# Optimization experiments

Measured on AMD Instinct MI355X. Metric: run time of the kernel, lower is better.

The kernel has to match this reference:

```python
import jax, jax.numpy as jnp
import numpy as np

D_MODEL = 256; N_HEADS = 8; HEAD_DIM = 32; N_LEVELS = 4; N_POINTS = 4; N_LAYERS = 3; D_FFN = 1024
SHAPES = np.array([[76, 76], [38, 38], [19, 19], [10, 10]], dtype=np.int64)
S_TOTAL = int((SHAPES[:, 0] * SHAPES[:, 1]).sum())  # 7681


def setup_inputs():
    key = jax.random.key(0)
    ks = jax.random.split(key, 12)
    B = 1; C = D_MODEL; M = N_HEADS; Lv = N_LEVELS; P = N_POINTS; L = N_LAYERS; s = 0.02
    starts = np.concatenate([[0], np.cumsum(SHAPES[:, 0] * SHAPES[:, 1])[:-1]]).astype(np.int64)
    inp = {
        "src": jax.random.normal(ks[0], (B, S_TOTAL, C), jnp.float32),
        "pos": jax.random.normal(ks[1], (B, S_TOTAL, C), jnp.float32),
        "valid_ratios": jnp.ones((B, Lv, 2), jnp.float32),
        "spatial_shapes": jnp.asarray(SHAPES),
        "level_start_index": jnp.asarray(starts),
        "padding_mask": jnp.zeros((B, S_TOTAL), bool),
        "W_off": jax.random.normal(ks[2], (L, C, M * Lv * P * 2), jnp.float32) * s,
        "b_off": jax.random.normal(ks[3], (L, M * Lv * P * 2), jnp.float32) * s,
        "W_attn": jax.random.normal(ks[4], (L, C, M * Lv * P), jnp.float32) * s,
        "b_attn": jax.random.normal(ks[5], (L, M * Lv * P), jnp.float32) * s,
        "W_val": jax.random.normal(ks[6], (L, C, C), jnp.float32) * s,
        "b_val": jnp.zeros((L, C), jnp.float32),
        "W_out": jax.random.normal(ks[7], (L, C, C), jnp.float32) * s,
        "b_out": jnp.zeros((L, C), jnp.float32),
        "ln1_g": jnp.ones((L, C), jnp.float32),
        "ln1_b": jnp.zeros((L, C), jnp.float32),
        "W_ff1": jax.random.normal(ks[8], (L, C, D_FFN), jnp.float32) * s,
        "b_ff1": jnp.zeros((L, D_FFN), jnp.float32),
        "W_ff2": jax.random.normal(ks[9], (L, D_FFN, C), jnp.float32) * s,
        "b_ff2": jnp.zeros((L, C), jnp.float32),
        "ln2_g": jnp.ones((L, C), jnp.float32),
        "ln2_b": jnp.zeros((L, C), jnp.float32),
    }
    return inp


def _ln(x, g, b):
    mu = x.mean(-1, keepdims=True)
    var = ((x - mu) ** 2).mean(-1, keepdims=True)
    return (x - mu) * jax.lax.rsqrt(var + 1e-5) * g + b


def _gather(v, idx):
    # v: [B, HW, M, D], idx: [B, S, M, P] -> [B, S, M, P, D], head-specific gather
    B, S, M, P = idx.shape
    def one(vb, ib):
        i2 = ib.transpose(0, 2, 1).reshape(S * P, M, 1)
        o = jnp.take_along_axis(vb, i2, axis=0)  # [S*P, M, D]
        return o.reshape(S, P, M, -1).transpose(0, 2, 1, 3)
    return jax.vmap(one)(v, idx)


def _msda(query, src, mask, ref, shapes, starts, Wo, bo, Wa, ba, Wv, bv, Wout, bout):
    # Multi-scale deformable attention (Deformable-DETR), grid_sample align_corners=False + zero padding
    B, S, C = src.shape
    M, Lv, P, D = N_HEADS, N_LEVELS, N_POINTS, HEAD_DIM
    value = src @ Wv + bv
    value = jnp.where(mask[..., None], 0.0, value).reshape(B, S, M, D)
    off = (query @ Wo + bo).reshape(B, S, M, Lv, P, 2)
    aw = jax.nn.softmax((query @ Wa + ba).reshape(B, S, M, Lv * P), -1).reshape(B, S, M, Lv, P)
    norm = jnp.asarray(shapes[:, ::-1].copy(), jnp.float32)  # (W, H) per level
    loc = ref[:, :, None, :, None, :] + off / norm[None, None, None, :, None, :]  # [B,S,M,Lv,P,2]
    out = jnp.zeros((B, S, M, D), query.dtype)
    for lvl in range(Lv):
        H = int(shapes[lvl, 0]); W = int(shapes[lvl, 1]); st = int(starts[lvl])
        v = value[:, st:st + H * W]  # [B, H*W, M, D]
        l = loc[:, :, :, lvl]  # [B, S, M, P, 2]
        x = l[..., 0] * W - 0.5
        y = l[..., 1] * H - 0.5
        x0 = jnp.floor(x); y0 = jnp.floor(y)
        dx = x - x0; dy = y - y0
        samp = jnp.zeros((B, S, M, P, D), query.dtype)
        for yy, xx, w in ((y0, x0, (1 - dy) * (1 - dx)), (y0, x0 + 1, (1 - dy) * dx),
                          (y0 + 1, x0, dy * (1 - dx)), (y0 + 1, x0 + 1, dy * dx)):
            valid = (xx >= 0) & (xx < W) & (yy >= 0) & (yy < H)
            xi = jnp.clip(xx, 0, W - 1).astype(jnp.int32)
            yi = jnp.clip(yy, 0, H - 1).astype(jnp.int32)
            g = _gather(v, yi * W + xi)
            samp = samp + (w * valid)[..., None] * g
        out = out + (aw[:, :, :, lvl, :, None] * samp).sum(3)
    return out.reshape(B, S, C) @ Wout + bout


def _ref_points(vr, shapes):
    refs = []
    for lvl in range(shapes.shape[0]):
        H = int(shapes[lvl, 0]); W = int(shapes[lvl, 1])
        ry, rx = np.meshgrid(np.linspace(0.5, H - 0.5, H, dtype=np.float32),
                             np.linspace(0.5, W - 0.5, W, dtype=np.float32), indexing="ij")
        rxj = jnp.asarray(rx.reshape(-1))[None] / (vr[:, None, lvl, 0] * W)
        ryj = jnp.asarray(ry.reshape(-1))[None] / (vr[:, None, lvl, 1] * H)
        refs.append(jnp.stack([rxj, ryj], -1))
    ref = jnp.concatenate(refs, 1)  # [B, S, 2]
    return ref[:, :, None] * vr[:, None]  # [B, S, Lv, 2]


def _encoder(src, pos, valid_ratios, shapes, starts, mask, params):
    (W_off, b_off, W_attn, b_attn, W_val, b_val, W_out, b_out,
     ln1_g, ln1_b, W_ff1, b_ff1, W_ff2, b_ff2, ln2_g, ln2_b) = params
    ref = _ref_points(valid_ratios, shapes)
    out = src
    for l in range(N_LAYERS):
        q = out + pos  # with_pos_embed
        a = _msda(q, out, mask, ref, shapes, starts, W_off[l], b_off[l], W_attn[l], b_attn[l],
                  W_val[l], b_val[l], W_out[l], b_out[l])
        out = _ln(out + a, ln1_g[l], ln1_b[l])
        f = jax.nn.relu(out @ W_ff1[l] + b_ff1[l]) @ W_ff2[l] + b_ff2[l]
        out = _ln(out + f, ln2_g[l], ln2_b[l])
    return out


def reference(src, pos, valid_ratios, spatial_shapes, level_start_index, padding_mask,
              W_off, b_off, W_attn, b_attn, W_val, b_val, W_out, b_out,
              ln1_g, ln1_b, W_ff1, b_ff1, W_ff2, b_ff2, ln2_g, ln2_b):
    shapes = np.asarray(spatial_shapes)
    starts = np.asarray(level_start_index)
    params = (W_off, b_off, W_attn, b_attn, W_val, b_val, W_out, b_out,
              ln1_g, ln1_b, W_ff1, b_ff1, W_ff2, b_ff2, ln2_g, ln2_b)
    return _encoder(src, pos, valid_ratios, shapes, starts, padding_mask, params)
```

## Files before the change

### kernel.cpp

```cpp
#include <hip/hip_runtime.h>
#include <hip/hip_bf16.h>
#include <math.h>

#define S_TOTAL 7681

typedef __attribute__((ext_vector_type(8))) short bf16x8;
typedef __attribute__((ext_vector_type(4))) float f32x4;

__device__ __forceinline__ short f2b(float x) {
    union { float f; unsigned u; } v; v.f = x;
    unsigned r = v.u + 0x7FFFu + ((v.u >> 16) & 1u);
    return (short)(r >> 16);
}
__device__ __forceinline__ float b2f(unsigned short u) {
    union { unsigned u; float f; } t; t.u = ((unsigned)u) << 16; return t.f;
}

__global__ __launch_bounds__(256) void transpose_cvt_kernel(
    const float* __restrict__ s0, const float* __restrict__ s1,
    const float* __restrict__ s2, const float* __restrict__ s3,
    const float* __restrict__ s4, const float* __restrict__ s5,
    short* __restrict__ d0, short* __restrict__ d1, short* __restrict__ d2,
    short* __restrict__ d3, short* __restrict__ d4, short* __restrict__ d5)
{
    const int z = blockIdx.z;
    int t = blockIdx.x;
    const float* src; short* dst; int K, N, lt;
    if (t < 64)       { src = s0 + (size_t)z * 65536;  dst = d0 + (size_t)z * 65536;  K = 256;  N = 256;  lt = t; }
    else if (t < 128) { src = s1 + (size_t)z * 65536;  dst = d1 + (size_t)z * 98304;  K = 256;  N = 256;  lt = t - 64; }
    else if (t < 160) { src = s2 + (size_t)z * 32768;  dst = d2 + (size_t)z * 98304;  K = 256;  N = 128;  lt = t - 128; }
    else if (t < 224) { src = s3 + (size_t)z * 65536;  dst = d3 + (size_t)z * 65536;  K = 256;  N = 256;  lt = t - 160; }
    else if (t < 480) { src = s4 + (size_t)z * 262144; dst = d4 + (size_t)z * 262144; K = 256;  N = 1024; lt = t - 224; }
    else              { src = s5 + (size_t)z * 262144; dst = d5 + (size_t)z * 262144; K = 1024; N = 256;  lt = t - 480; }
    const int ntx = N >> 5;
    const int tk = (lt / ntx) << 5, tn = (lt % ntx) << 5;
    __shared__ float tile[32][33];
    const int cx = threadIdx.x & 31, cy = threadIdx.x >> 5;
    #pragma unroll
    for (int i = 0; i < 32; i += 8)
        tile[cy + i][cx] = src[(size_t)(tk + cy + i) * N + tn + cx];
    __syncthreads();
    #pragma unroll
    for (int i = 0; i < 32; i += 8)
        dst[(size_t)(tn + cy + i) * K + tk + cx] = f2b(tile[cx][cy + i]);
}

__global__ void bias_cat_kernel(const float* __restrict__ b_off,
                                const float* __restrict__ b_attn,
                                float* __restrict__ b_oa) {
    int l = blockIdx.x, i = threadIdx.x;
    b_oa[l * 384 + i] = (i < 256) ? b_off[l * 256 + i] : b_attn[l * 128 + (i - 256)];
}

#define BM 128
#define BN 64
#define BK 32
#define KP 40

template<int RELU, int OUTBF>
__global__ __launch_bounds__(256) void gemm_kernel(
    const short* __restrict__ A, const short* __restrict__ Wt,
    const float* __restrict__ bias, void* __restrict__ Cv,
    int M, int N, int K)
{
    __shared__ __align__(16) short As[BM * KP];
    __shared__ __align__(16) short Bs[BN * KP];
    const int tid = threadIdx.x;
    const int lane = tid & 63;
    const int wave = tid >> 6;
    const int rowBase = blockIdx.x * BM;
    const int colBase = blockIdx.y * BN;

    const int ar = tid >> 1;
    const int ak = (tid & 1) * 16;
    const int br = tid >> 2;
    const int bk = (tid & 3) * 8;

    const int frow = lane & 15;
    const int fko  = (lane >> 4) * 8;
    const int wm = wave * 32;

    f32x4 acc[2][4] = {};

    const int aRow = rowBase + ar;
    const bool aOk = aRow < M;
    const short* Ap = A + (size_t)aRow * K + ak;
    const short* Bp = Wt + (size_t)(colBase + br) * K + bk;

    bf16x8 a0 = {}, a1 = {}, b0 = {};
    if (aOk) { a0 = *(const bf16x8*)Ap; a1 = *(const bf16x8*)(Ap + 8); }
    b0 = *(const bf16x8*)Bp;

    for (int k0 = 0; k0 < K; k0 += BK) {
        *(bf16x8*)&As[ar * KP + ak]     = a0;
        *(bf16x8*)&As[ar * KP + ak + 8] = a1;
        *(bf16x8*)&Bs[br * KP + bk]     = b0;
        __syncthreads();

        const int kn = k0 + BK;
        if (kn < K) {
            if (aOk) { a0 = *(const bf16x8*)(Ap + kn); a1 = *(const bf16x8*)(Ap + kn + 8); }
            b0 = *(const bf16x8*)(Bp + kn);
        }

        bf16x8 af0 = *(const bf16x8*)&As[(wm + frow) * KP + fko];
        bf16x8 af1 = *(const bf16x8*)&As[(wm + 16 + frow) * KP + fko];
        #pragma unroll
        for (int j = 0; j < 4; ++j) {
            bf16x8 bfj = *(const bf16x8*)&Bs[(j * 16 + frow) * KP + fko];
            acc[0][j] = __builtin_amdgcn_mfma_f32_16x16x32_bf16(af0, bfj, acc[0][j], 0, 0, 0);
            acc[1][j] = __builtin_amdgcn_mfma_f32_16x16x32_bf16(af1, bfj, acc[1][j], 0, 0, 0);
        }
        __syncthreads();
    }

    const int erow = (lane >> 4) * 4;
    const int ecol = lane & 15;
    #pragma unroll
    for (int mi = 0; mi < 2; ++mi) {
        #pragma unroll
        for (int j = 0; j < 4; ++j) {
            #pragma unroll
            for (int r = 0; r < 4; ++r) {
                int row = rowBase + wm + mi * 16 + erow + r;
                if (row < M) {
                    int col = colBase + j * 16 + ecol;
                    float v = acc[mi][j][r] + bias[col];
                    if (RELU) v = fmaxf(v, 0.f);
                    if (OUTBF) ((short*)Cv)[(size_t)row * N + col] = f2b(v);
                    else       ((float*)Cv)[(size_t)row * N + col] = v;
                }
            }
        }
    }
}

template<int WRITEQ>
__global__ __launch_bounds__(256) void gemm_ln_kernel(
    const short* __restrict__ A, const short* __restrict__ Wt,
    const float* __restrict__ bias, const float* __restrict__ g,
    const float* __restrict__ bln, const float* __restrict__ pos,
    float* __restrict__ out, short* __restrict__ xb, short* __restrict__ qb,
    int M, int K)
{
    __shared__ __align__(16) short As[32 * KP];
    __shared__ __align__(16) short Bs[256 * KP];
    __shared__ float rsum[32][4], rsq[32][4], smu[32], srs[32];

    const int tid = threadIdx.x;
    const int lane = tid & 63;
    const int wave = tid >> 6;
    const int rowBase = blockIdx.x * 32;

    const int frow = lane & 15;
    const int fko  = (lane >> 4) * 8;

    f32x4 acc[2][4] = {};

    const int ar = tid >> 1;
    const int ak = (tid & 1) * 16;
    const int aRow = rowBase + ar;
    const bool aOk = (tid < 64) && (aRow < M);
    const short* Ap = A + (size_t)aRow * K + ak;
    const short* Bp = Wt + (size_t)tid * K;

    bf16x8 a0 = {}, a1 = {};
    bf16x8 w0, w1, w2, w3;
    if (aOk) { a0 = *(const bf16x8*)Ap; a1 = *(const bf16x8*)(Ap + 8); }
    w0 = *(const bf16x8*)(Bp);      w1 = *(const bf16x8*)(Bp + 8);
    w2 = *(const bf16x8*)(Bp + 16); w3 = *(const bf16x8*)(Bp + 24);

    for (int k0 = 0; k0 < K; k0 += BK) {
        if (tid < 64) {
            *(bf16x8*)&As[ar * KP + ak]     = a0;
            *(bf16x8*)&As[ar * KP + ak + 8] = a1;
        }
        *(bf16x8*)&Bs[tid * KP + 0]  = w0;
        *(bf16x8*)&Bs[tid * KP + 8]  = w1;
        *(bf16x8*)&Bs[tid * KP + 16] = w2;
        *(bf16x8*)&Bs[tid * KP + 24] = w3;
        __syncthreads();

        const int kn = k0 + BK;
        if (kn < K) {
            if (aOk) { a0 = *(const bf16x8*)(Ap + kn); a1 = *(const bf16x8*)(Ap + kn + 8); }
            w0 = *(const bf16x8*)(Bp + kn);      w1 = *(const bf16x8*)(Bp + kn + 8);
            w2 = *(const bf16x8*)(Bp + kn + 16); w3 = *(const bf16x8*)(Bp + kn + 24);
        }

        bf16x8 af0 = *(const bf16x8*)&As[frow * KP + fko];
        bf16x8 af1 = *(const bf16x8*)&As[(16 + frow) * KP + fko];
        #pragma unroll
        for (int j = 0; j < 4; ++j) {
            bf16x8 bfj = *(const bf16x8*)&Bs[(wave * 64 + j * 16 + frow) * KP + fko];
            acc[0][j] = __builtin_amdgcn_mfma_f32_16x16x32_bf16(af0, bfj, acc[0][j], 0, 0, 0);
            acc[1][j] = __builtin_amdgcn_mfma_f32_16x16x32_bf16(af1, bfj, acc[1][j], 0, 0, 0);
        }
        __syncthreads();
    }

    const int erow = (lane >> 4) * 4;
    const int ecol = lane & 15;
    float x[2][4][4];
    #pragma unroll
    for (int mi = 0; mi < 2; ++mi)
        #pragma unroll
        for (int j = 0; j < 4; ++j)
            #pragma unroll
            for (int r = 0; r < 4; ++r) {
                int row = rowBase + mi * 16 + erow + r;
                int col = wave * 64 + j * 16 + ecol;
                float res = (row < M) ? out[(size_t)row * 256 + col] : 0.f;
                x[mi][j][r] = acc[mi][j][r] + bias[col] + res;
            }

    #pragma unroll
    for (int mi = 0; mi < 2; ++mi)
        #pragma unroll
        for (int r = 0; r < 4; ++r) {
            float s1 = x[mi][0][r] + x[mi][1][r] + x[mi][2][r] + x[mi][3][r];
            float s2 = x[mi][0][r]*x[mi][0][r] + x[mi][1][r]*x[mi][1][r]
                     + x[mi][2][r]*x[mi][2][r] + x[mi][3][r]*x[mi][3][r];
            #pragma unroll
            for (int o = 1; o < 16; o <<= 1) {
                s1 += __shfl_xor(s1, o);
                s2 += __shfl_xor(s2, o);
            }
            if ((lane & 15) == 0) {
                rsum[mi * 16 + erow + r][wave] = s1;
                rsq [mi * 16 + erow + r][wave] = s2;
            }
        }
    __syncthreads();
    if (tid < 32) {
        float S1 = rsum[tid][0] + rsum[tid][1] + rsum[tid][2] + rsum[tid][3];
        float S2 = rsq[tid][0] + rsq[tid][1] + rsq[tid][2] + rsq[tid][3];
        float mu = S1 * (1.f / 256.f);
        smu[tid] = mu;
        srs[tid] = rsqrtf(S2 * (1.f / 256.f) - mu * mu + 1e-5f);
    }
    __syncthreads();

    #pragma unroll
    for (int mi = 0; mi < 2; ++mi)
        #pragma unroll
        for (int r = 0; r < 4; ++r) {
            int lrow = mi * 16 + erow + r;
            int row = rowBase + lrow;
            if (row >= M) continue;
            float mu = smu[lrow], rs = srs[lrow];
            #pragma unroll
            for (int j = 0; j < 4; ++j) {
                int col = wave * 64 + j * 16 + ecol;
                float y = (x[mi][j][r] - mu) * rs * g[col] + bln[col];
                out[(size_t)row * 256 + col] = y;
                xb[(size_t)row * 256 + col] = f2b(y);
                if (WRITEQ)
                    qb[(size_t)row * 256 + col] = f2b(y + pos[(size_t)row * 256 + col]);
            }
        }
}

__global__ __launch_bounds__(256) void msda_kernel(
    const short* __restrict__ value, const float* __restrict__ offb,
    short* __restrict__ msdab)
{
    __shared__ float  soff[4 * 384];
    __shared__ int4   sIdx[512];
    __shared__ float4 sWgt[512];

    const int bid = blockIdx.x;
    const int sb = (bid & 7) * 241 + (bid >> 3);
    const int q0 = sb * 4;
    if (q0 >= S_TOTAL) return;
    const int tid = threadIdx.x;

    #pragma unroll
    for (int i = tid; i < 1536; i += 256) {
        int qi = i / 384, j = i - qi * 384;
        int q = min(q0 + qi, S_TOTAL - 1);
        soff[i] = offb[(size_t)q * 384 + j];
    }
    __syncthreads();

    if (tid < 32) {
        const int qi = tid >> 3, m = tid & 7;
        float* lg = &soff[qi * 384 + 256 + m * 16];
        float mx = -1e30f;
        #pragma unroll
        for (int k = 0; k < 16; ++k) mx = fmaxf(mx, lg[k]);
        float e[16], sum = 0.f;
        #pragma unroll
        for (int k = 0; k < 16; ++k) { e[k] = expf(lg[k] - mx); sum += e[k]; }
        float inv = 1.f / sum;
        #pragma unroll
        for (int k = 0; k < 16; ++k) lg[k] = e[k] * inv;
    }
    __syncthreads();

    #pragma unroll
    for (int it = tid; it < 512; it += 256) {
        const int qi = it >> 7, i = it & 127;
        const int lvl = (i >> 2) & 3;
        const int q = min(q0 + qi, S_TOTAL - 1);

        float refx, refy;
        if (q < 5776)      { int t = q;        int r = t / 76, c = t % 76; refx = (c + 0.5f) / 76.f; refy = (r + 0.5f) / 76.f; }
        else if (q < 7220) { int t = q - 5776; int r = t / 38, c = t % 38; refx = (c + 0.5f) / 38.f; refy = (r + 0.5f) / 38.f; }
        else if (q < 7581) { int t = q - 7220; int r = t / 19, c = t % 19; refx = (c + 0.5f) / 19.f; refy = (r + 0.5f) / 19.f; }
        else               { int t = q - 7581; int r = t / 10, c = t % 10; refx = (c + 0.5f) / 10.f; refy = (r + 0.5f) / 10.f; }

        const int LVL_HW[4] = {76, 38, 19, 10};
        const int LVL_ST[4] = {0, 5776, 7220, 7581};
        const int W = LVL_HW[lvl];
        const float fW = (float)W;

        float ox = soff[qi * 384 + i * 2];
        float oy = soff[qi * 384 + i * 2 + 1];
        float aw = soff[qi * 384 + 256 + i];

        float x = refx * fW + ox - 0.5f;
        float y = refy * fW + oy - 0.5f;
        float x0f = floorf(x), y0f = floorf(y);
        int x0 = (int)x0f, y0 = (int)y0f;
        float dx = x - x0f, dy = y - y0f;

        bool vx0 = (x0 >= 0) & (x0 < W);
        bool vx1 = (x0 >= -1) & (x0 < W - 1);
        bool vy0 = (y0 >= 0) & (y0 < W);
        bool vy1 = (y0 >= -1) & (y0 < W - 1);
        int xc0 = min(max(x0, 0), W - 1), xc1 = min(max(x0 + 1, 0), W - 1);
        int yc0 = min(max(y0, 0), W - 1), yc1 = min(max(y0 + 1, 0), W - 1);
        int base = LVL_ST[lvl];
        int4 id;
        id.x = base + yc0 * W + xc0;
        id.y = base + yc0 * W + xc1;
        id.z = base + yc1 * W + xc0;
        id.w = base + yc1 * W + xc1;
        float4 w4;
        w4.x = (vy0 && vx0) ? (1.f - dy) * (1.f - dx) * aw : 0.f;
        w4.y = (vy0 && vx1) ? (1.f - dy) * dx * aw : 0.f;
        w4.z = (vy1 && vx0) ? dy * (1.f - dx) * aw : 0.f;
        w4.w = (vy1 && vx1) ? dy * dx * aw : 0.f;
        sIdx[it] = id;
        sWgt[it] = w4;
    }
    __syncthreads();

    const int qi = tid >> 6;
    const int q = q0 + qi;
    if (q >= S_TOTAL) return;
    const int lane = tid & 63;
    const int h = lane >> 3, d4 = lane & 7;
    const short* vcol = value + h * 32 + d4 * 4;

    float a0 = 0.f, a1 = 0.f, a2 = 0.f, a3 = 0.f;
    #pragma unroll
    for (int pt = 0; pt < 16; ++pt) {
        const int it = qi * 128 + (h << 4) + pt;
        const int4 id = sIdx[it];
        const float4 w = sWgt[it];
        ushort4 v0 = *(const ushort4*)(vcol + ((size_t)id.x << 8));
        ushort4 v1 = *(const ushort4*)(vcol + ((size_t)id.y << 8));
        ushort4 v2 = *(const ushort4*)(vcol + ((size_t)id.z << 8));
        ushort4 v3 = *(const ushort4*)(vcol + ((size_t)id.w << 8));
        a0 += w.x * b2f(v0.x) + w.y * b2f(v1.x) + w.z * b2f(v2.x) + w.w * b2f(v3.x);
        a1 += w.x * b2f(v0.y) + w.y * b2f(v1.y) + w.z * b2f(v2.y) + w.w * b2f(v3.y);
        a2 += w.x * b2f(v0.z) + w.y * b2f(v1.z) + w.z * b2f(v2.z) + w.w * b2f(v3.z);
        a3 += w.x * b2f(v0.w) + w.y * b2f(v1.w) + w.z * b2f(v2.w) + w.w * b2f(v3.w);
    }
    ushort4 o;
    o.x = (unsigned short)f2b(a0); o.y = (unsigned short)f2b(a1);
    o.z = (unsigned short)f2b(a2); o.w = (unsigned short)f2b(a3);
    *(ushort4*)(msdab + (size_t)q * 256 + h * 32 + d4 * 4) = o;
}

__global__ __launch_bounds__(256) void cvt_copy_kernel(
    const float4* __restrict__ src, const float4* __restrict__ pos,
    float4* __restrict__ o, ushort4* __restrict__ xb, ushort4* __restrict__ qb,
    int n4)
{
    int i = blockIdx.x * blockDim.x + threadIdx.x;
    if (i < n4) {
        float4 v = src[i], p = pos[i];
        o[i] = v;
        ushort4 h, hq;
        h.x = (unsigned short)f2b(v.x); h.y = (unsigned short)f2b(v.y);
        h.z = (unsigned short)f2b(v.z); h.w = (unsigned short)f2b(v.w);
        hq.x = (unsigned short)f2b(v.x + p.x); hq.y = (unsigned short)f2b(v.y + p.y);
        hq.z = (unsigned short)f2b(v.z + p.z); hq.w = (unsigned short)f2b(v.w + p.w);
        xb[i] = h;
        qb[i] = hq;
    }
}

extern "C" void kernel_launch(void* const* d_in, const int* in_sizes, int n_in,
                              void* d_out, int out_size, void* d_ws, size_t ws_size,
                              hipStream_t stream) {
    const float* src    = (const float*)d_in[0];
    const float* pos    = (const float*)d_in[1];
    const float* W_off  = (const float*)d_in[6];
    const float* b_off  = (const float*)d_in[7];
    const float* W_attn = (const float*)d_in[8];
    const float* b_attn = (const float*)d_in[9];
    const float* W_val  = (const float*)d_in[10];
    const float* b_val  = (const float*)d_in[11];
    const float* W_out  = (const float*)d_in[12];
    const float* b_out  = (const float*)d_in[13];
    const float* ln1_g  = (const float*)d_in[14];
    const float* ln1_b  = (const float*)d_in[15];
    const float* W_ff1  = (const float*)d_in[16];
    const float* b_ff1  = (const float*)d_in[17];
    const float* W_ff2  = (const float*)d_in[18];
    const float* b_ff2  = (const float*)d_in[19];
    const float* ln2_g  = (const float*)d_in[20];
    const float* ln2_b  = (const float*)d_in[21];

    const size_t S = S_TOTAL;
    float* out = (float*)d_out;

    short* wt = (short*)d_ws;
    short* Wt_val = wt;
    short* Wt_oa  = wt + 196608;
    short* Wt_out = wt + 491520;
    short* Wt_ff1 = wt + 688128;
    short* Wt_ff2 = wt + 1474560;
    float* b_oa   = (float*)d_ws + 1130496;
    float* fbase  = (float*)d_ws + 1131648;
    short* xb       = (short*)fbase;
    short* qb       = (short*)(fbase + 128 * S);
    short* value_bf = (short*)(fbase + 256 * S);
    float* offb     = fbase + 384 * S;
    short* msdab    = (short*)(fbase + 768 * S);
    short* hid      = (short*)(fbase + 256 * S);

    transpose_cvt_kernel<<<dim3(736, 1, 3), 256, 0, stream>>>(
        W_val, W_off, W_attn, W_out, W_ff1, W_ff2,
        Wt_val, Wt_oa, Wt_oa + 65536, Wt_out, Wt_ff1, Wt_ff2);
    bias_cat_kernel<<<3, 384, 0, stream>>>(b_off, b_attn, b_oa);

    const int n4 = (int)(S * 256 / 4);
    const int g4 = (n4 + 255) / 256;
    cvt_copy_kernel<<<g4, 256, 0, stream>>>((const float4*)src, (const float4*)pos,
                                            (float4*)out, (ushort4*)xb, (ushort4*)qb, n4);

    const int MB = (S_TOTAL + BM - 1) / BM;
    const int LB = (S_TOTAL + 31) / 32;

    for (int l = 0; l < 3; ++l) {
        gemm_kernel<0, 1><<<dim3(MB, 4), 256, 0, stream>>>(
            xb, Wt_val + (size_t)l * 65536, b_val + (size_t)l * 256, value_bf,
            S_TOTAL, 256, 256);
        gemm_kernel<0, 0><<<dim3(MB, 6), 256, 0, stream>>>(
            qb, Wt_oa + (size_t)l * 98304, b_oa + (size_t)l * 384, offb,
            S_TOTAL, 384, 256);
        msda_kernel<<<1928, 256, 0, stream>>>(value_bf, offb, msdab);
        gemm_ln_kernel<0><<<LB, 256, 0, stream>>>(
            msdab, Wt_out + (size_t)l * 65536, b_out + (size_t)l * 256,
            ln1_g + (size_t)l * 256, ln1_b + (size_t)l * 256, pos,
            out, xb, qb, S_TOTAL, 256);
        gemm_kernel<1, 1><<<dim3(MB, 16), 256, 0, stream>>>(
            xb, Wt_ff1 + (size_t)l * 262144, b_ff1 + (size_t)l * 1024, hid,
            S_TOTAL, 1024, 256);
        gemm_ln_kernel<1><<<LB, 256, 0, stream>>>(
            hid, Wt_ff2 + (size_t)l * 262144, b_ff2 + (size_t)l * 256,
            ln2_g + (size_t)l * 256, ln2_b + (size_t)l * 256, pos,
            out, xb, qb, S_TOTAL, 1024);
    }
}
```

Measured before the change: 451.6 us.

## Merge value and offset GEMMs into one launch; widen MSDA gathers to 8 queries

Replaces the separate value-projection and offset/attention GEMM launches with a single kernel whose grid y-dimension selects the problem, reading biases directly and dropping the bias concatenation kernel. The MSDA kernel now handles 8 queries per block, stores sampling indices as 16-bit values, loads offsets with float4, and gathers 8 bf16 channels per lane instead of 4. These aim to cut launch overhead, shrink shared memory for indices, and improve gather width and memory-level parallelism. The trade-off is fewer MSDA blocks and higher register use per lane.

```diff
diff --git a/kernel.cpp b/kernel.cpp
--- a/kernel.cpp
+++ b/kernel.cpp
@@ -45,17 +45,95 @@
         dst[(size_t)(tn + cy + i) * K + tk + cx] = f2b(tile[cx][cy + i]);
 }
 
-__global__ void bias_cat_kernel(const float* __restrict__ b_off,
-                                const float* __restrict__ b_attn,
-                                float* __restrict__ b_oa) {
-    int l = blockIdx.x, i = threadIdx.x;
-    b_oa[l * 384 + i] = (i < 256) ? b_off[l * 256 + i] : b_attn[l * 128 + (i - 256)];
-}
-
 #define BM 128
 #define BN 64
 #define BK 32
 #define KP 40
+
+__global__ __launch_bounds__(256) void gemm_va_kernel(
+    const short* __restrict__ xb, const short* __restrict__ qb,
+    const short* __restrict__ Wt_val, const short* __restrict__ Wt_oa,
+    const float* __restrict__ b_val, const float* __restrict__ b_off,
+    const float* __restrict__ b_attn,
+    short* __restrict__ value_bf, float* __restrict__ offbuf, int M)
+{
+    const int grp = (blockIdx.y >= 4);
+    const short* A  = grp ? qb : xb;
+    const short* Wt = grp ? Wt_oa : Wt_val;
+    const int colBase = (grp ? (blockIdx.y - 4) : blockIdx.y) * BN;
+    const int N = grp ? 384 : 256;
+    const int K = 256;
+
+    __shared__ __align__(16) short As[BM * KP];
+    __shared__ __align__(16) short Bs[BN * KP];
+    const int tid = threadIdx.x;
+    const int lane = tid & 63;
+    const int wave = tid >> 6;
+    const int rowBase = blockIdx.x * BM;
+
+    const int ar = tid >> 1;
+    const int ak = (tid & 1) * 16;
+    const int br = tid >> 2;
+    const int bk = (tid & 3) * 8;
+
+    const int frow = lane & 15;
+    const int fko  = (lane >> 4) * 8;
+    const int wm = wave * 32;
+
+    f32x4 acc[2][4] = {};
+
+    const int aRow = rowBase + ar;
+    const bool aOk = aRow < M;
+    const short* Ap = A + (size_t)aRow * K + ak;
+    const short* Bp = Wt + (size_t)(colBase + br) * K + bk;
+
+    bf16x8 a0 = {}, a1 = {}, b0 = {};
+    if (aOk) { a0 = *(const bf16x8*)Ap; a1 = *(const bf16x8*)(Ap + 8); }
+    b0 = *(const bf16x8*)Bp;
+
+    for (int k0 = 0; k0 < K; k0 += BK) {
+        *(bf16x8*)&As[ar * KP + ak]     = a0;
+        *(bf16x8*)&As[ar * KP + ak + 8] = a1;
+        *(bf16x8*)&Bs[br * KP + bk]     = b0;
+        __syncthreads();
+
+        const int kn = k0 + BK;
+        if (kn < K) {
+            if (aOk) { a0 = *(const bf16x8*)(Ap + kn); a1 = *(const bf16x8*)(Ap + kn + 8); }
+            b0 = *(const bf16x8*)(Bp + kn);
+        }
+
+        bf16x8 af0 = *(const bf16x8*)&As[(wm + frow) * KP + fko];
+        bf16x8 af1 = *(const bf16x8*)&As[(wm + 16 + frow) * KP + fko];
+        #pragma unroll
+        for (int j = 0; j < 4; ++j) {
+            bf16x8 bfj = *(const bf16x8*)&Bs[(j * 16 + frow) * KP + fko];
+            acc[0][j] = __builtin_amdgcn_mfma_f32_16x16x32_bf16(af0, bfj, acc[0][j], 0, 0, 0);
+            acc[1][j] = __builtin_amdgcn_mfma_f32_16x16x32_bf16(af1, bfj, acc[1][j], 0, 0, 0);
+        }
+        __syncthreads();
+    }
+
+    const int erow = (lane >> 4) * 4;
+    const int ecol = lane & 15;
+    #pragma unroll
+    for (int mi = 0; mi < 2; ++mi) {
+        #pragma unroll
+        for (int j = 0; j < 4; ++j) {
+            int col = colBase + j * 16 + ecol;
+            float bias = grp ? (col < 256 ? b_off[col] : b_attn[col - 256]) : b_val[col];
+            #pragma unroll
+            for (int r = 0; r < 4; ++r) {
+                int row = rowBase + wm + mi * 16 + erow + r;
+                if (row < M) {
+                    float v = acc[mi][j][r] + bias;
+                    if (grp) offbuf[(size_t)row * 384 + col] = v;
+                    else     value_bf[(size_t)row * 256 + col] = f2b(v);
+                }
+            }
+        }
+    }
+}
 
 template<int RELU, int OUTBF>
 __global__ __launch_bounds__(256) void gemm_kernel(
@@ -265,25 +343,28 @@
     const short* __restrict__ value, const float* __restrict__ offb,
     short* __restrict__ msdab)
 {
-    __shared__ float  soff[4 * 384];
-    __shared__ int4   sIdx[512];
-    __shared__ float4 sWgt[512];
+    __shared__ float   soff[8 * 384];
+    __shared__ ushort4 sIdx[1024];
+    __shared__ float4  sWgt[1024];
 
     const int bid = blockIdx.x;
-    const int sb = (bid & 7) * 241 + (bid >> 3);
-    const int q0 = sb * 4;
+    const int sb = (bid & 7) * 121 + (bid >> 3);
+    const int q0 = sb * 8;
     if (q0 >= S_TOTAL) return;
     const int tid = threadIdx.x;
 
-    #pragma unroll
-    for (int i = tid; i < 1536; i += 256) {
-        int qi = i / 384, j = i - qi * 384;
-        int q = min(q0 + qi, S_TOTAL - 1);
-        soff[i] = offb[(size_t)q * 384 + j];
+    {
+        const float4* src4 = (const float4*)offb;
+        #pragma unroll
+        for (int i = tid; i < 768; i += 256) {
+            int qi = i / 96, j = i - qi * 96;
+            int q = min(q0 + qi, S_TOTAL - 1);
+            *(float4*)&soff[qi * 384 + j * 4] = src4[(size_t)q * 96 + j];
+        }
     }
     __syncthreads();
 
-    if (tid < 32) {
+    if (tid < 64) {
         const int qi = tid >> 3, m = tid & 7;
         float* lg = &soff[qi * 384 + 256 + m * 16];
         float mx = -1e30f;
@@ -299,7 +380,7 @@
     __syncthreads();
 
     #pragma unroll
-    for (int it = tid; it < 512; it += 256) {
+    for (int it = tid; it < 1024; it += 256) {
         const int qi = it >> 7, i = it & 127;
         const int lvl = (i >> 2) & 3;
         const int q = min(q0 + qi, S_TOTAL - 1);
@@ -332,11 +413,11 @@
         int xc0 = min(max(x0, 0), W - 1), xc1 = min(max(x0 + 1, 0), W - 1);
         int yc0 = min(max(y0, 0), W - 1), yc1 = min(max(y0 + 1, 0), W - 1);
         int base = LVL_ST[lvl];
-        int4 id;
-        id.x = base + yc0 * W + xc0;
-        id.y = base + yc0 * W + xc1;
-        id.z = base + yc1 * W + xc0;
-        id.w = base + yc1 * W + xc1;
+        ushort4 id;
+        id.x = (unsigned short)(base + yc0 * W + xc0);
+        id.y = (unsigned short)(base + yc0 * W + xc1);
+        id.z = (unsigned short)(base + yc1 * W + xc0);
+        id.w = (unsigned short)(base + yc1 * W + xc1);
         float4 w4;
         w4.x = (vy0 && vx0) ? (1.f - dy) * (1.f - dx) * aw : 0.f;
         w4.y = (vy0 && vx1) ? (1.f - dy) * dx * aw : 0.f;
@@ -347,32 +428,33 @@
     }
     __syncthreads();
 
-    const int qi = tid >> 6;
+    const int lane = tid & 63;
+    const int qi = (tid >> 6) * 2 + (lane >> 5);
     const int q = q0 + qi;
     if (q >= S_TOTAL) return;
-    const int lane = tid & 63;
-    const int h = lane >> 3, d4 = lane & 7;
-    const short* vcol = value + h * 32 + d4 * 4;
-
-    float a0 = 0.f, a1 = 0.f, a2 = 0.f, a3 = 0.f;
+    const int l32 = lane & 31;
+    const int h = l32 >> 2, dg = l32 & 3;
+    const short* vcol = value + h * 32 + dg * 8;
+    const int itb = qi * 128 + (h << 4);
+
+    float a[8] = {};
     #pragma unroll
     for (int pt = 0; pt < 16; ++pt) {
-        const int it = qi * 128 + (h << 4) + pt;
-        const int4 id = sIdx[it];
-        const float4 w = sWgt[it];
-        ushort4 v0 = *(const ushort4*)(vcol + ((size_t)id.x << 8));
-        ushort4 v1 = *(const ushort4*)(vcol + ((size_t)id.y << 8));
-        ushort4 v2 = *(const ushort4*)(vcol + ((size_t)id.z << 8));
-        ushort4 v3 = *(const ushort4*)(vcol + ((size_t)id.w << 8));
-        a0 += w.x * b2f(v0.x) + w.y * b2f(v1.x) + w.z * b2f(v2.x) + w.w * b2f(v3.x);
-        a1 += w.x * b2f(v0.y) + w.y * b2f(v1.y) + w.z * b2f(v2.y) + w.w * b2f(v3.y);
-        a2 += w.x * b2f(v0.z) + w.y * b2f(v1.z) + w.z * b2f(v2.z) + w.w * b2f(v3.z);
-        a3 += w.x * b2f(v0.w) + w.y * b2f(v1.w) + w.z * b2f(v2.w) + w.w * b2f(v3.w);
-    }
-    ushort4 o;
-    o.x = (unsigned short)f2b(a0); o.y = (unsigned short)f2b(a1);
-    o.z = (unsigned short)f2b(a2); o.w = (unsigned short)f2b(a3);
-    *(ushort4*)(msdab + (size_t)q * 256 + h * 32 + d4 * 4) = o;
+        const ushort4 id = sIdx[itb + pt];
+        const float4 w = sWgt[itb + pt];
+        bf16x8 v0 = *(const bf16x8*)(vcol + ((size_t)id.x << 8));
+        bf16x8 v1 = *(const bf16x8*)(vcol + ((size_t)id.y << 8));
+        bf16x8 v2 = *(const bf16x8*)(vcol + ((size_t)id.z << 8));
+        bf16x8 v3 = *(const bf16x8*)(vcol + ((size_t)id.w << 8));
+        #pragma unroll
+        for (int e = 0; e < 8; ++e)
+            a[e] += w.x * b2f((unsigned short)v0[e]) + w.y * b2f((unsigned short)v1[e])
+                  + w.z * b2f((unsigned short)v2[e]) + w.w * b2f((unsigned short)v3[e]);
+    }
+    bf16x8 o;
+    #pragma unroll
+    for (int e = 0; e < 8; ++e) o[e] = f2b(a[e]);
+    *(bf16x8*)(msdab + (size_t)q * 256 + h * 32 + dg * 8) = o;
 }
 
 __global__ __launch_bounds__(256) void cvt_copy_kernel(
@@ -425,7 +507,6 @@
     short* Wt_out = wt + 491520;
     short* Wt_ff1 = wt + 688128;
     short* Wt_ff2 = wt + 1474560;
-    float* b_oa   = (float*)d_ws + 1130496;
     float* fbase  = (float*)d_ws + 1131648;
     short* xb       = (short*)fbase;
     short* qb       = (short*)(fbase + 128 * S);
@@ -437,7 +518,6 @@
     transpose_cvt_kernel<<<dim3(736, 1, 3), 256, 0, stream>>>(
         W_val, W_off, W_attn, W_out, W_ff1, W_ff2,
         Wt_val, Wt_oa, Wt_oa + 65536, Wt_out, Wt_ff1, Wt_ff2);
-    bias_cat_kernel<<<3, 384, 0, stream>>>(b_off, b_attn, b_oa);
 
     const int n4 = (int)(S * 256 / 4);
     const int g4 = (n4 + 255) / 256;
@@ -448,13 +528,11 @@
     const int LB = (S_TOTAL + 31) / 32;
 
     for (int l = 0; l < 3; ++l) {
-        gemm_kernel<0, 1><<<dim3(MB, 4), 256, 0, stream>>>(
-            xb, Wt_val + (size_t)l * 65536, b_val + (size_t)l * 256, value_bf,
-            S_TOTAL, 256, 256);
-        gemm_kernel<0, 0><<<dim3(MB, 6), 256, 0, stream>>>(
-            qb, Wt_oa + (size_t)l * 98304, b_oa + (size_t)l * 384, offb,
-            S_TOTAL, 384, 256);
-        msda_kernel<<<1928, 256, 0, stream>>>(value_bf, offb, msdab);
+        gemm_va_kernel<<<dim3(MB, 10), 256, 0, stream>>>(
+            xb, qb, Wt_val + (size_t)l * 65536, Wt_oa + (size_t)l * 98304,
+            b_val + (size_t)l * 256, b_off + (size_t)l * 256, b_attn + (size_t)l * 128,
+            value_bf, offb, S_TOTAL);
+        msda_kernel<<<968, 256, 0, stream>>>(value_bf, offb, msdab);
         gemm_ln_kernel<0><<<LB, 256, 0, stream>>>(
             msdab, Wt_out + (size_t)l * 65536, b_out + (size_t)l * 256,
             ln1_g + (size_t)l * 256, ln1_b + (size_t)l * 256, pos,
```

After: 415.8 us. 1.09x faster.
